# Kernel tuning notes

Hardware: AMD Instinct MI355X
Metric: run time of the kernel (lower is better)

Reference implementation:

```python
import jax, jax.numpy as jnp
import numpy as np

N, C, A, CI = 32768, 512, 64, 1024  # n_locations, content_size, address_size, controller_input_size
EPS = 1e-7


def setup_inputs() -> dict:
    key = jax.random.key(0)
    ks = jax.random.split(key, 12)
    g = lambda i, shape, s=1.0: jax.random.normal(ks[i], shape, dtype=jnp.float32) * s
    xav = lambda i, shape: g(i, shape, float(np.sqrt(2.0 / (shape[0] + shape[1]))))
    return {
        "controller_hidden_state": g(0, (N, 1)),
        "controller_input": g(1, (CI, 1)),
        "memory_contents": g(2, (N, C), 0.5),
        "memory_addresses": xav(3, (N, A)),
        "exp_mov_avg_similarity": g(4, (N, 1), 0.1),
        "W_query": xav(5, (C + A, N)),
        "b_query": jnp.zeros((C + A, 1), jnp.float32),
        "u_sharpen": xav(6, (1, N)),
        "b_sharpen": jnp.zeros((1,), jnp.float32),
        "u_lru": xav(7, (1, N)),
        "b_lru": jnp.zeros((1,), jnp.float32),
        "W_erase": xav(8, (C, N)),
        "b_erase": jnp.zeros((C, 1), jnp.float32),
        "W_content_hidden": xav(9, (C, N)),
        "W_content_input": xav(10, (C, CI)),
        "u_content_alpha": xav(11, (N + CI, 1)),
        "b_content_alpha": jnp.zeros((1, 1), jnp.float32),
    }


def reference(controller_hidden_state, controller_input, memory_contents, memory_addresses,
              exp_mov_avg_similarity, W_query, b_query, u_sharpen, b_sharpen, u_lru, b_lru,
              W_erase, b_erase, W_content_hidden, W_content_input, u_content_alpha,
              b_content_alpha):
    h, x = controller_hidden_state, controller_input
    # ---- address_memory ----
    full_mem = jnp.concatenate([memory_addresses, memory_contents], axis=1)  # [N, A+C]
    query = W_query @ h + b_query                                            # [A+C, 1]
    beta = jax.nn.softplus(u_sharpen @ h + b_sharpen) + 1.0                  # [1, 1]
    q = query[:, 0]
    q_norm = jnp.maximum(jnp.linalg.norm(q), EPS)
    m_norm = jnp.maximum(jnp.linalg.norm(full_mem, axis=1), EPS)             # [N]
    cos = (full_mem @ q) / (m_norm * q_norm)                                 # [N] cosine sim per location
    sim = (beta[0, 0] * cos)[:, None]                                        # [N, 1]
    gamma = jax.nn.sigmoid(u_lru @ h + b_lru)                                # [1, 1] LRU gate
    addr = jax.nn.softmax(sim - gamma * exp_mov_avg_similarity, axis=0)      # [N, 1]
    # (state buffer update, next-step only): new_ema = 0.1*ema + 0.9*sim
    # ---- update (vectorized erase/write over all N locations) ----
    erase = W_erase @ h + b_erase                                            # [C, 1]
    alpha = u_content_alpha.T @ jnp.concatenate([h, x], axis=0) + b_content_alpha  # [1, 1]
    cand = jax.nn.relu(W_content_hidden @ h + alpha * (W_content_input @ x))       # [C, 1]
    new_mem = (1.0 - addr * erase.T) * memory_contents + addr * cand.T       # [N, C]
    # ---- read (on updated memory) ----
    new_full = jnp.concatenate([memory_addresses, new_mem], axis=1)          # [N, A+C]
    read = new_full.T @ addr                                                 # [A+C, 1]
    return read
```

## Files before the change

kernel.cpp:

```cpp
#include <hip/hip_runtime.h>
#include <hip/hip_bf16.h>
#include <math.h>

#define NN 32768
#define CC 512
#define AA 64
#define CIN 1024
#define EPSV 1e-7f


__global__ __launch_bounds__(256) void k1_gemv(
    const float* __restrict__ h, const float* __restrict__ x,
    const float* __restrict__ Wq, const float* __restrict__ bq,
    const float* __restrict__ ush, const float* __restrict__ ulr,
    const float* __restrict__ Wer, const float* __restrict__ ber,
    const float* __restrict__ Wch, const float* __restrict__ Wci,
    const float* __restrict__ uca,
    float* __restrict__ ws)
{
    __shared__ float red[256];
    const int r = blockIdx.x, tid = threadIdx.x;
    float sum = 0.f;
    if (r < 1600 || r >= 2112) {
        const float* vec;
        if (r < 576)       vec = Wq  + (size_t)r * NN;
        else if (r < 1088) vec = Wer + (size_t)(r - 576) * NN;
        else if (r < 1600) vec = Wch + (size_t)(r - 1088) * NN;
        else if (r == 2112) vec = ush;
        else if (r == 2113) vec = ulr;
        else                vec = uca;
        for (int j = tid * 4; j < NN; j += 1024) {
            float4 a = *reinterpret_cast<const float4*>(vec + j);
            float4 b = *reinterpret_cast<const float4*>(h + j);
            sum += a.x * b.x + a.y * b.y + a.z * b.z + a.w * b.w;
        }
        if (r == 2114) {
            float4 a = *reinterpret_cast<const float4*>(uca + NN + tid * 4);
            float4 b = *reinterpret_cast<const float4*>(x + tid * 4);
            sum += a.x * b.x + a.y * b.y + a.z * b.z + a.w * b.w;
        }
    } else {
        const float* vec = Wci + (size_t)(r - 1600) * CIN;
        float4 a = *reinterpret_cast<const float4*>(vec + tid * 4);
        float4 b = *reinterpret_cast<const float4*>(x + tid * 4);
        sum += a.x * b.x + a.y * b.y + a.z * b.z + a.w * b.w;
    }
    red[tid] = sum; __syncthreads();
    for (int st = 128; st > 0; st >>= 1) {
        if (tid < st) red[tid] += red[tid + st];
        __syncthreads();
    }
    if (tid == 0) {
        float v = red[0];
        if (r < 576)       v += bq[r];
        else if (r < 1088) v += ber[r - 576];
        ws[r] = v;
    }
}

__global__ __launch_bounds__(256) void k1b_scalars(
    const float* __restrict__ bsh, const float* __restrict__ blr,
    const float* __restrict__ bca, float* __restrict__ ws)
{
    __shared__ float red[256];
    const int tid = threadIdx.x;
    float s = 0.f;
    for (int j = tid; j < 576; j += 256) { float q = ws[j]; s += q * q; }
    red[tid] = s; __syncthreads();
    for (int st = 128; st > 0; st >>= 1) {
        if (tid < st) red[tid] += red[tid + st];
        __syncthreads();
    }
    if (tid == 0) {
        float qn = fmaxf(sqrtf(red[0]), EPSV);
        float bp = ws[2112] + bsh[0];
        float beta = (bp > 20.f ? bp : log1pf(expf(bp))) + 1.0f;
        float gp = ws[2113] + blr[0];
        float gamma = 1.f / (1.f + expf(-gp));
        float alpha = ws[2114] + bca[0];
        ws[2112] = beta; ws[2113] = gamma; ws[2114] = alpha; ws[2115] = qn;
    }
}

__global__ __launch_bounds__(256) void k2_sim(
    const float* __restrict__ Mm, const float* __restrict__ Ad,
    const float* __restrict__ ema, const float* __restrict__ ws,
    float* __restrict__ ws_s)
{
    const int tid = threadIdx.x, wave = tid >> 6, lane = tid & 63;
    const float beta = ws[2112], gamma = ws[2113], qn = ws[2115];
    const float ql = ws[lane];
    float4 qa = *reinterpret_cast<const float4*>(ws + 64 + lane * 8);
    float4 qb = *reinterpret_cast<const float4*>(ws + 68 + lane * 8);
    float qm[8] = {qa.x, qa.y, qa.z, qa.w, qb.x, qb.y, qb.z, qb.w};
    #pragma unroll
    for (int j = 0; j < 4; ++j) {
        const int i = blockIdx.x * 16 + wave * 4 + j;
        float a = Ad[(size_t)i * AA + lane];
        float4 m0 = *reinterpret_cast<const float4*>(Mm + (size_t)i * CC + lane * 8);
        float4 m1 = *reinterpret_cast<const float4*>(Mm + (size_t)i * CC + lane * 8 + 4);
        float mm[8] = {m0.x, m0.y, m0.z, m0.w, m1.x, m1.y, m1.z, m1.w};
        float dot = a * ql, nn = a * a;
        #pragma unroll
        for (int k = 0; k < 8; ++k) { float f = mm[k]; dot += f * qm[k]; nn += f * f; }
        #pragma unroll
        for (int off = 32; off >= 1; off >>= 1) {
            dot += __shfl_xor(dot, off);
            nn  += __shfl_xor(nn, off);
        }
        if (lane == 0) {
            float mn = fmaxf(sqrtf(nn), EPSV);
            ws_s[i] = beta * (dot / (mn * qn)) - gamma * ema[i];
        }
    }
}

__global__ __launch_bounds__(1024) void k3_softmax(float* __restrict__ ws)
{
    const float* s = ws + 2128;
    __shared__ float lmx[16], lz[16], ls2[16], bc[1];
    const int tid = threadIdx.x, lane = tid & 63, wid = tid >> 6;
    float v[32];
    float mx = -1e30f;
    #pragma unroll
    for (int j = 0; j < 32; ++j) { v[j] = s[tid + 1024 * j]; mx = fmaxf(mx, v[j]); }
    #pragma unroll
    for (int off = 32; off >= 1; off >>= 1) mx = fmaxf(mx, __shfl_xor(mx, off));
    if (lane == 0) lmx[wid] = mx;
    __syncthreads();
    if (tid == 0) { float m = lmx[0]; for (int k = 1; k < 16; ++k) m = fmaxf(m, lmx[k]); bc[0] = m; }
    __syncthreads();
    mx = bc[0];
    float z = 0.f, s2 = 0.f;
    #pragma unroll
    for (int j = 0; j < 32; ++j) { float e = expf(v[j] - mx); z += e; s2 += e * e; }
    #pragma unroll
    for (int off = 32; off >= 1; off >>= 1) { z += __shfl_xor(z, off); s2 += __shfl_xor(s2, off); }
    if (lane == 0) { lz[wid] = z; ls2[wid] = s2; }
    __syncthreads();
    if (tid == 0) {
        float Z = 0.f, S = 0.f;
        for (int k = 0; k < 16; ++k) { Z += lz[k]; S += ls2[k]; }
        ws[2116] = mx; ws[2117] = 1.f / Z; ws[2118] = S / (Z * Z);
    }
}

__global__ __launch_bounds__(256) void k4_acc(
    const float* __restrict__ Mm, const float* __restrict__ Ad,
    const float* __restrict__ ws, float* __restrict__ pm, float* __restrict__ pa)
{
    __shared__ float lds[4][1024];
    const int b = blockIdx.x, tid = threadIdx.x, wave = tid >> 6, lane = tid & 63;
    const float* s = ws + 2128;
    const float mx = ws[2116], invZ = ws[2117];
    if (b < 512) {
        float a1[8] = {0,0,0,0,0,0,0,0};
        float a2[8] = {0,0,0,0,0,0,0,0};
        for (int j = 0; j < 16; ++j) {
            const int i = b * 64 + j * 4 + wave;
            float w1 = expf(s[i] - mx) * invZ;
            float w2 = w1 * w1;
            float4 m0 = *reinterpret_cast<const float4*>(Mm + (size_t)i * CC + lane * 8);
            float4 m1 = *reinterpret_cast<const float4*>(Mm + (size_t)i * CC + lane * 8 + 4);
            float mm[8] = {m0.x, m0.y, m0.z, m0.w, m1.x, m1.y, m1.z, m1.w};
            #pragma unroll
            for (int k = 0; k < 8; ++k) { float f = mm[k]; a1[k] += w1 * f; a2[k] += w2 * f; }
        }
        #pragma unroll
        for (int k = 0; k < 8; ++k) {
            lds[wave][lane * 8 + k] = a1[k];
            lds[wave][512 + lane * 8 + k] = a2[k];
        }
        __syncthreads();
        for (int e = tid; e < 1024; e += 256) {
            float v = lds[0][e] + lds[1][e] + lds[2][e] + lds[3][e];
            pm[(size_t)e * 512 + b] = v;
        }
    } else {
        const int bb = b - 512;
        float acc = 0.f;
        for (int j = 0; j < 64; ++j) {
            const int i = bb * 256 + j * 4 + wave;
            float w1 = expf(s[i] - mx) * invZ;
            acc += w1 * Ad[(size_t)i * AA + lane];
        }
        lds[wave][lane] = acc;
        __syncthreads();
        if (tid < 64) {
            float v = lds[0][tid] + lds[1][tid] + lds[2][tid] + lds[3][tid];
            pa[tid * 128 + bb] = v;
        }
    }
}

__global__ __launch_bounds__(256) void k5_final(
    const float* __restrict__ ws, const float* __restrict__ pm,
    const float* __restrict__ pa, float* __restrict__ out)
{
    __shared__ float red[256];
    const int b = blockIdx.x, tid = threadIdx.x;
    if (b < 64) {
        float v = (tid < 128) ? pa[b * 128 + tid] : 0.f;
        red[tid] = v; __syncthreads();
        for (int st = 128; st > 0; st >>= 1) {
            if (tid < st) red[tid] += red[tid + st];
            __syncthreads();
        }
        if (tid == 0) out[b] = red[0];
    } else {
        const int c = b - 64;
        float v1 = pm[(size_t)c * 512 + tid] + pm[(size_t)c * 512 + tid + 256];
        float v2 = pm[(size_t)(512 + c) * 512 + tid] + pm[(size_t)(512 + c) * 512 + tid + 256];
        red[tid] = v1; __syncthreads();
        for (int st = 128; st > 0; st >>= 1) {
            if (tid < st) red[tid] += red[tid + st];
            __syncthreads();
        }
        float s1 = red[0];
        __syncthreads();
        red[tid] = v2; __syncthreads();
        for (int st = 128; st > 0; st >>= 1) {
            if (tid < st) red[tid] += red[tid + st];
            __syncthreads();
        }
        if (tid == 0) {
            float s2v = red[0];
            float er = ws[576 + c], ch = ws[1088 + c], cx = ws[1600 + c];
            float alpha = ws[2114], S2 = ws[2118];
            float cand = fmaxf(ch + alpha * cx, 0.f);
            out[64 + c] = s1 - er * s2v + S2 * cand;
        }
    }
}

extern "C" void kernel_launch(void* const* d_in, const int* in_sizes, int n_in,
                              void* d_out, int out_size, void* d_ws, size_t ws_size,
                              hipStream_t stream)
{
    const float* h   = (const float*)d_in[0];
    const float* x   = (const float*)d_in[1];
    const float* Mm  = (const float*)d_in[2];
    const float* Ad  = (const float*)d_in[3];
    const float* ema = (const float*)d_in[4];
    const float* Wq  = (const float*)d_in[5];
    const float* bq  = (const float*)d_in[6];
    const float* ush = (const float*)d_in[7];
    const float* bsh = (const float*)d_in[8];
    const float* ulr = (const float*)d_in[9];
    const float* blr = (const float*)d_in[10];
    const float* Wer = (const float*)d_in[11];
    const float* ber = (const float*)d_in[12];
    const float* Wch = (const float*)d_in[13];
    const float* Wci = (const float*)d_in[14];
    const float* uca = (const float*)d_in[15];
    const float* bca = (const float*)d_in[16];

    float* ws   = (float*)d_ws;
    float* ws_s = ws + 2128;
    float* pm   = ws + 34896;
    float* pa   = ws + 559184;
    float* out  = (float*)d_out;

    hipLaunchKernelGGL(k1_gemv,    dim3(2115), dim3(256),  0, stream,
                       h, x, Wq, bq, ush, ulr, Wer, ber, Wch, Wci, uca, ws);
    hipLaunchKernelGGL(k1b_scalars, dim3(1),   dim3(256),  0, stream, bsh, blr, bca, ws);
    hipLaunchKernelGGL(k2_sim,     dim3(2048), dim3(256),  0, stream, Mm, Ad, ema, ws, ws_s);
    hipLaunchKernelGGL(k3_softmax, dim3(1),    dim3(1024), 0, stream, ws);
    hipLaunchKernelGGL(k4_acc,     dim3(640),  dim3(256),  0, stream, Mm, Ad, ws, pm, pa);
    hipLaunchKernelGGL(k5_final,   dim3(576),  dim3(256),  0, stream, ws, pm, pa, out);
}
```

Baseline: 326.7 us.

## Restructure GEMV to process 8 rows per block with split-K atomics

The large GEMV kernel now has each block compute 8 weight rows over a 4096-wide chunk of h. The h chunk is staged in shared memory and reused across rows, and partial sums are combined with atomicAdd into a workspace that is zeroed by a memset. Biases are now added in later kernels, and the query vector is copied to a new workspace offset. The aim is more memory-level parallelism and better bandwidth on the roughly 200MB weight stream, at the cost of an extra memset and atomics whose accumulation order is nondeterministic.

```diff
diff --git a/kernel.cpp b/kernel.cpp
--- a/kernel.cpp
+++ b/kernel.cpp
@@ -9,63 +9,130 @@
 #define EPSV 1e-7f
 
 
+#define QOFF 2128
+#define SOFF 2704
+#define PMOFF 35472
+#define PAOFF 559760
+
 __global__ __launch_bounds__(256) void k1_gemv(
     const float* __restrict__ h, const float* __restrict__ x,
-    const float* __restrict__ Wq, const float* __restrict__ bq,
+    const float* __restrict__ Wq, const float* __restrict__ Wer,
+    const float* __restrict__ Wch, const float* __restrict__ Wci,
     const float* __restrict__ ush, const float* __restrict__ ulr,
-    const float* __restrict__ Wer, const float* __restrict__ ber,
-    const float* __restrict__ Wch, const float* __restrict__ Wci,
-    const float* __restrict__ uca,
+    const float* __restrict__ uca, float* __restrict__ ws)
+{
+    const int b = blockIdx.x, tid = threadIdx.x;
+    const int wave = tid >> 6, lane = tid & 63;
+    __shared__ float hs[4096];
+    __shared__ float red[4][8];
+
+    if (b < 1600) {
+        const int rg = b >> 3, chunk = b & 7;
+        const float4* h4 = reinterpret_cast<const float4*>(h) + chunk * 1024;
+        float4* hs4 = reinterpret_cast<float4*>(hs);
+        #pragma unroll
+        for (int k = 0; k < 4; ++k) hs4[k * 256 + tid] = h4[k * 256 + tid];
+        __syncthreads();
+        const int r0 = rg * 8;
+        const float* mat; int base;
+        if (r0 < 576)       { mat = Wq;  base = 0; }
+        else if (r0 < 1088) { mat = Wer; base = 576; }
+        else                { mat = Wch; base = 1088; }
+        const float4* m4 = reinterpret_cast<const float4*>(
+            mat + (size_t)(r0 - base) * NN + chunk * 4096);
+        const int rs = NN / 4;
+        float acc[8] = {0,0,0,0,0,0,0,0};
+        #pragma unroll
+        for (int it = 0; it < 4; ++it) {
+            float4 hb = hs4[it * 256 + tid];
+            #pragma unroll
+            for (int r = 0; r < 8; ++r) {
+                float4 a = m4[(size_t)r * rs + it * 256 + tid];
+                acc[r] += a.x * hb.x + a.y * hb.y + a.z * hb.z + a.w * hb.w;
+            }
+        }
+        #pragma unroll
+        for (int r = 0; r < 8; ++r) {
+            #pragma unroll
+            for (int off = 32; off >= 1; off >>= 1)
+                acc[r] += __shfl_xor(acc[r], off);
+        }
+        if (lane == 0) {
+            #pragma unroll
+            for (int r = 0; r < 8; ++r) red[wave][r] = acc[r];
+        }
+        __syncthreads();
+        if (tid < 8) {
+            float v = red[0][tid] + red[1][tid] + red[2][tid] + red[3][tid];
+            atomicAdd(ws + r0 + tid, v);
+        }
+    } else if (b < 1664) {
+        const int rg = b - 1600;
+        float4 xv = reinterpret_cast<const float4*>(x)[tid];
+        const float4* m4 = reinterpret_cast<const float4*>(
+            Wci + (size_t)rg * 8 * CIN);
+        float acc[8];
+        #pragma unroll
+        for (int r = 0; r < 8; ++r) {
+            float4 a = m4[r * 256 + tid];
+            acc[r] = a.x * xv.x + a.y * xv.y + a.z * xv.z + a.w * xv.w;
+        }
+        #pragma unroll
+        for (int r = 0; r < 8; ++r) {
+            #pragma unroll
+            for (int off = 32; off >= 1; off >>= 1)
+                acc[r] += __shfl_xor(acc[r], off);
+        }
+        if (lane == 0) {
+            #pragma unroll
+            for (int r = 0; r < 8; ++r) red[wave][r] = acc[r];
+        }
+        __syncthreads();
+        if (tid < 8) {
+            float v = red[0][tid] + red[1][tid] + red[2][tid] + red[3][tid];
+            ws[1600 + rg * 8 + tid] = v;
+        }
+    } else {
+        const int t = b - 1664, sd = t >> 3, chunk = t & 7;
+        const float* vec = (sd == 0) ? ush : (sd == 1) ? ulr : uca;
+        const float4* v4 = reinterpret_cast<const float4*>(vec) + chunk * 1024;
+        const float4* h4 = reinterpret_cast<const float4*>(h) + chunk * 1024;
+        float acc = 0.f;
+        #pragma unroll
+        for (int it = 0; it < 4; ++it) {
+            float4 a = v4[it * 256 + tid];
+            float4 hb = h4[it * 256 + tid];
+            acc += a.x * hb.x + a.y * hb.y + a.z * hb.z + a.w * hb.w;
+        }
+        if (sd == 2 && chunk == 0) {
+            float4 a = reinterpret_cast<const float4*>(uca)[NN / 4 + tid];
+            float4 xv = reinterpret_cast<const float4*>(x)[tid];
+            acc += a.x * xv.x + a.y * xv.y + a.z * xv.z + a.w * xv.w;
+        }
+        #pragma unroll
+        for (int off = 32; off >= 1; off >>= 1)
+            acc += __shfl_xor(acc, off);
+        if (lane == 0) red[wave][0] = acc;
+        __syncthreads();
+        if (tid == 0)
+            atomicAdd(ws + 2112 + sd,
+                      red[0][0] + red[1][0] + red[2][0] + red[3][0]);
+    }
+}
+
+__global__ __launch_bounds__(256) void k1b_scalars(
+    const float* __restrict__ bq, const float* __restrict__ bsh,
+    const float* __restrict__ blr, const float* __restrict__ bca,
     float* __restrict__ ws)
-{
-    __shared__ float red[256];
-    const int r = blockIdx.x, tid = threadIdx.x;
-    float sum = 0.f;
-    if (r < 1600 || r >= 2112) {
-        const float* vec;
-        if (r < 576)       vec = Wq  + (size_t)r * NN;
-        else if (r < 1088) vec = Wer + (size_t)(r - 576) * NN;
-        else if (r < 1600) vec = Wch + (size_t)(r - 1088) * NN;
-        else if (r == 2112) vec = ush;
-        else if (r == 2113) vec = ulr;
-        else                vec = uca;
-        for (int j = tid * 4; j < NN; j += 1024) {
-            float4 a = *reinterpret_cast<const float4*>(vec + j);
-            float4 b = *reinterpret_cast<const float4*>(h + j);
-            sum += a.x * b.x + a.y * b.y + a.z * b.z + a.w * b.w;
-        }
-        if (r == 2114) {
-            float4 a = *reinterpret_cast<const float4*>(uca + NN + tid * 4);
-            float4 b = *reinterpret_cast<const float4*>(x + tid * 4);
-            sum += a.x * b.x + a.y * b.y + a.z * b.z + a.w * b.w;
-        }
-    } else {
-        const float* vec = Wci + (size_t)(r - 1600) * CIN;
-        float4 a = *reinterpret_cast<const float4*>(vec + tid * 4);
-        float4 b = *reinterpret_cast<const float4*>(x + tid * 4);
-        sum += a.x * b.x + a.y * b.y + a.z * b.z + a.w * b.w;
-    }
-    red[tid] = sum; __syncthreads();
-    for (int st = 128; st > 0; st >>= 1) {
-        if (tid < st) red[tid] += red[tid + st];
-        __syncthreads();
-    }
-    if (tid == 0) {
-        float v = red[0];
-        if (r < 576)       v += bq[r];
-        else if (r < 1088) v += ber[r - 576];
-        ws[r] = v;
-    }
-}
-
-__global__ __launch_bounds__(256) void k1b_scalars(
-    const float* __restrict__ bsh, const float* __restrict__ blr,
-    const float* __restrict__ bca, float* __restrict__ ws)
 {
     __shared__ float red[256];
     const int tid = threadIdx.x;
     float s = 0.f;
-    for (int j = tid; j < 576; j += 256) { float q = ws[j]; s += q * q; }
+    for (int j = tid; j < 576; j += 256) {
+        float q = ws[j] + bq[j];
+        ws[QOFF + j] = q;
+        s += q * q;
+    }
     red[tid] = s; __syncthreads();
     for (int st = 128; st > 0; st >>= 1) {
         if (tid < st) red[tid] += red[tid + st];
@@ -89,9 +156,9 @@
 {
     const int tid = threadIdx.x, wave = tid >> 6, lane = tid & 63;
     const float beta = ws[2112], gamma = ws[2113], qn = ws[2115];
-    const float ql = ws[lane];
-    float4 qa = *reinterpret_cast<const float4*>(ws + 64 + lane * 8);
-    float4 qb = *reinterpret_cast<const float4*>(ws + 68 + lane * 8);
+    const float ql = ws[QOFF + lane];
+    float4 qa = *reinterpret_cast<const float4*>(ws + QOFF + 64 + lane * 8);
+    float4 qb = *reinterpret_cast<const float4*>(ws + QOFF + 68 + lane * 8);
     float qm[8] = {qa.x, qa.y, qa.z, qa.w, qb.x, qb.y, qb.z, qb.w};
     #pragma unroll
     for (int j = 0; j < 4; ++j) {
@@ -117,7 +184,7 @@
 
 __global__ __launch_bounds__(1024) void k3_softmax(float* __restrict__ ws)
 {
-    const float* s = ws + 2128;
+    const float* s = ws + SOFF;
     __shared__ float lmx[16], lz[16], ls2[16], bc[1];
     const int tid = threadIdx.x, lane = tid & 63, wid = tid >> 6;
     float v[32];
@@ -151,7 +218,7 @@
 {
     __shared__ float lds[4][1024];
     const int b = blockIdx.x, tid = threadIdx.x, wave = tid >> 6, lane = tid & 63;
-    const float* s = ws + 2128;
+    const float* s = ws + SOFF;
     const float mx = ws[2116], invZ = ws[2117];
     if (b < 512) {
         float a1[8] = {0,0,0,0,0,0,0,0};
@@ -195,7 +262,8 @@
 
 __global__ __launch_bounds__(256) void k5_final(
     const float* __restrict__ ws, const float* __restrict__ pm,
-    const float* __restrict__ pa, float* __restrict__ out)
+    const float* __restrict__ pa, const float* __restrict__ ber,
+    float* __restrict__ out)
 {
     __shared__ float red[256];
     const int b = blockIdx.x, tid = threadIdx.x;
@@ -225,7 +293,8 @@
         }
         if (tid == 0) {
             float s2v = red[0];
-            float er = ws[576 + c], ch = ws[1088 + c], cx = ws[1600 + c];
+            float er = ws[576 + c] + ber[c];
+            float ch = ws[1088 + c], cx = ws[1600 + c];
             float alpha = ws[2114], S2 = ws[2118];
             float cand = fmaxf(ch + alpha * cx, 0.f);
             out[64 + c] = s1 - er * s2v + S2 * cand;
@@ -256,16 +325,19 @@
     const float* bca = (const float*)d_in[16];
 
     float* ws   = (float*)d_ws;
-    float* ws_s = ws + 2128;
-    float* pm   = ws + 34896;
-    float* pa   = ws + 559184;
+    float* ws_s = ws + SOFF;
+    float* pm   = ws + PMOFF;
+    float* pa   = ws + PAOFF;
     float* out  = (float*)d_out;
 
-    hipLaunchKernelGGL(k1_gemv,    dim3(2115), dim3(256),  0, stream,
-                       h, x, Wq, bq, ush, ulr, Wer, ber, Wch, Wci, uca, ws);
-    hipLaunchKernelGGL(k1b_scalars, dim3(1),   dim3(256),  0, stream, bsh, blr, bca, ws);
+    hipMemsetAsync(ws, 0, QOFF * sizeof(float), stream);
+
+    hipLaunchKernelGGL(k1_gemv,    dim3(1688), dim3(256),  0, stream,
+                       h, x, Wq, Wer, Wch, Wci, ush, ulr, uca, ws);
+    hipLaunchKernelGGL(k1b_scalars, dim3(1),   dim3(256),  0, stream,
+                       bq, bsh, blr, bca, ws);
     hipLaunchKernelGGL(k2_sim,     dim3(2048), dim3(256),  0, stream, Mm, Ad, ema, ws, ws_s);
     hipLaunchKernelGGL(k3_softmax, dim3(1),    dim3(1024), 0, stream, ws);
     hipLaunchKernelGGL(k4_acc,     dim3(640),  dim3(256),  0, stream, Mm, Ad, ws, pm, pa);
-    hipLaunchKernelGGL(k5_final,   dim3(576),  dim3(256),  0, stream, ws, pm, pa, out);
-}
+    hipLaunchKernelGGL(k5_final,   dim3(576),  dim3(256),  0, stream, ws, pm, pa, ber, out);
+}
```

After: 330.2 us. No clear change (+1.1%).
